# Kernel optimization log

Hardware: AMD Instinct MI355X
Metric: run time of the kernel (lower is better)

Reference implementation:

```python
import jax, jax.numpy as jnp
import numpy as np

B, L, IN_DIM, D_MODEL = 4, 1024, 128, 256
MDIM = 2 * D_MODEL          # mamba_dim = 512 (must equal 2*d_model for shape consistency)
NL = 4                      # mamba_layers
DIN = 2 * MDIM              # d_inner (expand=2)
NST = 16                    # d_state
DTR = MDIM // 16            # dt_rank = 32
KC = 4                      # d_conv
EPS = 1e-5

# sinusoidal positional encoding buffer (deterministic)
_pos = np.arange(L, dtype=np.float32)[:, None]
_div = np.exp(np.arange(0, MDIM, 2, dtype=np.float32) * (-np.log(10000.0) / MDIM))
_pe = np.zeros((L, MDIM), dtype=np.float32)
_pe[:, 0::2] = np.sin(_pos * _div)
_pe[:, 1::2] = np.cos(_pos * _div)
PE = jnp.asarray(_pe)


def setup_inputs() -> dict:
    key = jax.random.key(0)
    ks = iter(jax.random.split(key, 64))
    rn = lambda shape, s=0.02: jax.random.normal(next(ks), shape, jnp.float32) * s
    inp = {
        "x": jax.random.normal(next(ks), (B, L, IN_DIM), jnp.float32),
        "rtg": jax.random.normal(next(ks), (B, L, 1), jnp.float32),
        "state_emb_w": rn((D_MODEL, IN_DIM)), "state_emb_b": jnp.zeros((D_MODEL,)),
        "reward_emb_w": rn((D_MODEL, 1)), "reward_emb_b": jnp.zeros((D_MODEL,)),
        "ln_w": jnp.ones((MDIM,)), "ln_b": jnp.zeros((MDIM,)),
        "in_proj_w": rn((NL, 2 * DIN, MDIM)),
        "conv_w": rn((NL, DIN, KC), 0.1), "conv_b": jnp.zeros((NL, DIN)),
        "x_proj_w": rn((NL, DTR + 2 * NST, DIN)),
        "dt_proj_w": rn((NL, DIN, DTR), 0.1), "dt_proj_b": jnp.full((NL, DIN), -2.0),
        "A_log": jnp.tile(jnp.log(jnp.arange(1, NST + 1, dtype=jnp.float32)), (NL, DIN, 1)),
        "D_param": jnp.ones((NL, DIN)),
        "out_proj_w": rn((NL, MDIM, DIN)),
        "norm_w": jnp.ones((NL, MDIM)), "norm_f_w": jnp.ones((MDIM,)),
        "so_w1": rn((MDIM // 2, MDIM)), "so_b1": jnp.zeros((MDIM // 2,)),
        "so_w2": rn((IN_DIM, MDIM // 2)), "so_b2": jnp.zeros((IN_DIM,)),
        "ro_w1": rn((MDIM // 2, MDIM)), "ro_b1": jnp.zeros((MDIM // 2,)),
        "ro_w2": rn((1, MDIM // 2)), "ro_b2": jnp.zeros((1,)),
    }
    return inp


def _rmsnorm(h, w):
    return h * jax.lax.rsqrt(jnp.mean(h * h, -1, keepdims=True) + EPS) * w


def _mamba(h, ipw, cw, cb, xpw, dpw, dpb, Alog, Dp, opw):
    # h: [B,L,MDIM]
    Ls = h.shape[1]
    xz = h @ ipw.T                                   # [B,L,2*DIN]
    xx, z = jnp.split(xz, 2, axis=-1)
    # causal depthwise conv, kernel KC, left pad KC-1
    xp = jnp.pad(xx, ((0, 0), (KC - 1, 0), (0, 0)))
    xc = cb + sum(cw[:, k] * xp[:, k:k + Ls, :] for k in range(KC))
    xc = jax.nn.silu(xc)                             # [B,L,DIN]
    dbc = xc @ xpw.T                                 # [B,L,DTR+2*NST]
    dt = jax.nn.softplus(dbc[..., :DTR] @ dpw.T + dpb)   # [B,L,DIN]
    Bm = dbc[..., DTR:DTR + NST]                     # [B,L,NST]
    Cm = dbc[..., DTR + NST:]                        # [B,L,NST]
    A = -jnp.exp(Alog)                               # [DIN,NST]

    def step(hc, inp):
        dt_t, B_t, C_t, x_t = inp                    # [B,DIN],[B,NST],[B,NST],[B,DIN]
        hc = jnp.exp(dt_t[:, :, None] * A) * hc + (dt_t * x_t)[:, :, None] * B_t[:, None, :]
        return hc, jnp.einsum('bdn,bn->bd', hc, C_t)

    h0 = jnp.zeros((h.shape[0], DIN, NST), h.dtype)
    _, ys = jax.lax.scan(step, h0, (dt.swapaxes(0, 1), Bm.swapaxes(0, 1),
                                    Cm.swapaxes(0, 1), xc.swapaxes(0, 1)))
    y = ys.swapaxes(0, 1) + Dp * xc
    y = y * jax.nn.silu(z)
    return y @ opw.T                                 # [B,L,MDIM]


def _forward(x, rtg, state_emb_w, state_emb_b, reward_emb_w, reward_emb_b, ln_w, ln_b,
             in_proj_w, conv_w, conv_b, x_proj_w, dt_proj_w, dt_proj_b, A_log, D_param,
             out_proj_w, norm_w, norm_f_w, so_w1, so_b1, so_w2, so_b2, ro_w1, ro_b1, ro_w2, ro_b2):
    se = x @ state_emb_w.T + state_emb_b            # [B,L,D_MODEL]
    re = rtg @ reward_emb_w.T + reward_emb_b        # [B,L,D_MODEL]
    h = jnp.concatenate([se, re], axis=-1)          # [B,L,MDIM]
    h = h + PE[:h.shape[1]]                          # dropout is identity at eval
    mu = jnp.mean(h, -1, keepdims=True)
    var = jnp.var(h, -1, keepdims=True)
    h = (h - mu) * jax.lax.rsqrt(var + EPS) * ln_w + ln_b
    residual = None
    for i in range(NL):
        residual = h if residual is None else h + residual
        hn = _rmsnorm(residual, norm_w[i])
        h = _mamba(hn, in_proj_w[i], conv_w[i], conv_b[i], x_proj_w[i],
                   dt_proj_w[i], dt_proj_b[i], A_log[i], D_param[i], out_proj_w[i])
    residual = h + residual
    h = _rmsnorm(residual, norm_f_w)
    next_state = jax.nn.relu(h @ so_w1.T + so_b1) @ so_w2.T + so_b2   # [B,L,IN_DIM]
    next_reward = jax.nn.relu(h @ ro_w1.T + ro_b1) @ ro_w2.T + ro_b2  # [B,L,1]
    return next_state, next_reward


def reference(x, rtg, state_emb_w, state_emb_b, reward_emb_w, reward_emb_b, ln_w, ln_b,
              in_proj_w, conv_w, conv_b, x_proj_w, dt_proj_w, dt_proj_b, A_log, D_param,
              out_proj_w, norm_w, norm_f_w, so_w1, so_b1, so_w2, so_b2, ro_w1, ro_b1, ro_w2, ro_b2):
    return _forward(x, rtg, state_emb_w, state_emb_b, reward_emb_w, reward_emb_b, ln_w, ln_b,
                    in_proj_w, conv_w, conv_b, x_proj_w, dt_proj_w, dt_proj_b, A_log, D_param,
                    out_proj_w, norm_w, norm_f_w, so_w1, so_b1, so_w2, so_b2, ro_w1, ro_b1, ro_w2, ro_b2)
```

## Files before the change

### kernel.cpp

```cpp
#include <hip/hip_runtime.h>
#include <stdint.h>

typedef unsigned short u16;
typedef __attribute__((ext_vector_type(8))) short bf16x8;
typedef __attribute__((ext_vector_type(8))) u16 u16x8;
typedef __attribute__((ext_vector_type(4))) float f32x4;

static __device__ __forceinline__ u16 f2b(float f) {
  uint32_t u = __builtin_bit_cast(uint32_t, f);
  u += 0x7fffu + ((u >> 16) & 1u);
  return (u16)(u >> 16);
}
static __device__ __forceinline__ float b2f(u16 h) {
  uint32_t u = ((uint32_t)h) << 16;
  return __builtin_bit_cast(float, u);
}

#define GLDS16(gsrc, ldst)                                                        \
  __builtin_amdgcn_global_load_lds(                                               \
      (const __attribute__((address_space(1))) void*)(gsrc),                      \
      (__attribute__((address_space(3))) void*)(ldst), 16, 0, 0)

__global__ __launch_bounds__(256) void setup_kernel(
    const float* __restrict__ ipw, u16* __restrict__ ipwb,
    const float* __restrict__ xpw, u16* __restrict__ xpwb,
    const float* __restrict__ opw, u16* __restrict__ opwb,
    const float* __restrict__ sow1, u16* __restrict__ sow1b,
    const float* __restrict__ sow2, u16* __restrict__ sow2b,
    const float* __restrict__ row1, u16* __restrict__ row1b,
    float* __restrict__ PEt,
    const float* __restrict__ dpw, float* __restrict__ dpwT,
    const float* __restrict__ cw, float* __restrict__ cwT) {
  int i = blockIdx.x * 256 + threadIdx.x;
  if (i < 4194304) { ipwb[i] = f2b(ipw[i]); return; } i -= 4194304;
  if (i < 262144)  { xpwb[i] = f2b(xpw[i]); return; } i -= 262144;
  if (i < 2097152) { opwb[i] = f2b(opw[i]); return; } i -= 2097152;
  if (i < 131072)  { sow1b[i] = f2b(sow1[i]); return; } i -= 131072;
  if (i < 32768)   { sow2b[i] = f2b(sow2[i]); return; } i -= 32768;
  if (i < 131072)  { row1b[i] = f2b(row1[i]); return; } i -= 131072;
  if (i < 524288) {
    int dd = i & 511, l = i >> 9;
    const float cc = -9.210340371976184f / 512.f;
    float div = expf((float)(2 * (dd >> 1)) * cc);
    PEt[i] = (dd & 1) ? cosf((float)l * div) : sinf((float)l * div);
    return;
  } i -= 524288;
  if (i < 131072) {
    int l = i >> 15, r = i & 32767, j = r >> 10, dd = r & 1023;
    dpwT[i] = dpw[(size_t)l * 32768 + (size_t)dd * 32 + j];
    return;
  } i -= 131072;
  if (i < 16384) {
    int l = i >> 12, r = i & 4095, k = r >> 10, dd = r & 1023;
    cwT[i] = cw[(size_t)l * 4096 + (size_t)dd * 4 + k];
  }
}

__global__ __launch_bounds__(256) void embed_ln2(
    const float* __restrict__ x, const float* __restrict__ rtg,
    const float* __restrict__ Wse, const float* __restrict__ bse,
    const float* __restrict__ Wre, const float* __restrict__ bre,
    const float* __restrict__ lnw, const float* __restrict__ lnb,
    const float* __restrict__ PEt, float* __restrict__ h) {
  const int tid = threadIdx.x;
  const int tok0 = blockIdx.x * 16;
  const int l0 = tok0 & 1023;
  __shared__ float xs[16][128];
  __shared__ float rt[16];
  __shared__ float sw[16][2][4];
  for (int i = tid; i < 16 * 128; i += 256) ((float*)xs)[i] = x[(size_t)tok0 * 128 + i];
  if (tid < 16) rt[tid] = rtg[tok0 + tid];
  __syncthreads();
  const int d = tid;
  float acc[16];
#pragma unroll
  for (int tt = 0; tt < 16; ++tt) acc[tt] = 0.f;
  const float* wrow = Wse + (size_t)d * 128;
  for (int k0 = 0; k0 < 128; k0 += 8) {
    float4 wa = *(const float4*)(wrow + k0);
    float4 wb = *(const float4*)(wrow + k0 + 4);
#pragma unroll
    for (int tt = 0; tt < 16; ++tt) {
      const float* xr = &xs[tt][k0];
      acc[tt] += xr[0] * wa.x + xr[1] * wa.y + xr[2] * wa.z + xr[3] * wa.w +
                 xr[4] * wb.x + xr[5] * wb.y + xr[6] * wb.z + xr[7] * wb.w;
    }
  }
  const float seb = bse[d], reW = Wre[d], reB = bre[d];
  const int lane = tid & 63, wv = tid >> 6;
  float h1a[16];
#pragma unroll
  for (int tt = 0; tt < 16; ++tt) {
    float h0 = acc[tt] + seb + PEt[(size_t)(l0 + tt) * 512 + d];
    float h1 = reB + rt[tt] * reW + PEt[(size_t)(l0 + tt) * 512 + 256 + d];
    acc[tt] = h0;
    h1a[tt] = h1;
    float s = h0 + h1, q = h0 * h0 + h1 * h1;
#pragma unroll
    for (int o = 32; o; o >>= 1) { s += __shfl_xor(s, o); q += __shfl_xor(q, o); }
    if (lane == 0) { sw[tt][0][wv] = s; sw[tt][1][wv] = q; }
  }
  __syncthreads();
#pragma unroll
  for (int tt = 0; tt < 16; ++tt) {
    float S = sw[tt][0][0] + sw[tt][0][1] + sw[tt][0][2] + sw[tt][0][3];
    float Q = sw[tt][1][0] + sw[tt][1][1] + sw[tt][1][2] + sw[tt][1][3];
    float mean = S * (1.f / 512.f);
    float var = Q * (1.f / 512.f) - mean * mean;
    float rstd = rsqrtf(var + 1e-5f);
    size_t base = (size_t)(tok0 + tt) * 512;
    h[base + d]       = (acc[tt] - mean) * rstd * lnw[d] + lnb[d];
    h[base + 256 + d] = (h1a[tt] - mean) * rstd * lnw[256 + d] + lnb[256 + d];
  }
}

__global__ __launch_bounds__(256) void resid_rms_kernel(
    const float* __restrict__ hin, float* __restrict__ residual,
    const float* __restrict__ w, u16* __restrict__ outb, int first) {
  const int tok = blockIdx.x;
  const int t = threadIdx.x;
  __shared__ float rq[4];
  size_t base = (size_t)tok * 512;
  float v0 = hin[base + t], v1 = hin[base + t + 256];
  if (!first) { v0 += residual[base + t]; v1 += residual[base + t + 256]; }
  residual[base + t] = v0;
  residual[base + t + 256] = v1;
  float q = v0 * v0 + v1 * v1;
#pragma unroll
  for (int o = 32; o; o >>= 1) q += __shfl_xor(q, o);
  if ((t & 63) == 0) rq[t >> 6] = q;
  __syncthreads();
  float Q = rq[0] + rq[1] + rq[2] + rq[3];
  float scale = rsqrtf(Q * (1.f / 512.f) + 1e-5f);
  outb[base + t]       = f2b(v0 * scale * w[t]);
  outb[base + t + 256] = f2b(v1 * scale * w[t + 256]);
}

template <int BM, int BN, int WM, int WN, int EPI>
__global__ __launch_bounds__(256) void gemm_bt(
    const u16* __restrict__ A, const u16* __restrict__ Bw,
    float* __restrict__ Cf, u16* __restrict__ Cb,
    const float* __restrict__ bias, const float* __restrict__ bias2,
    int M, int N, int K, int As) {
  constexpr int MF = BM / (WM * 16);
  constexpr int NF = BN / (WN * 16);
  constexpr int NCA = (BM * 4) / 256;
  constexpr int NCB = (BN * 4) / 256;
  __shared__ __align__(16) u16 lA[BM * 32];
  __shared__ __align__(16) u16 lB[BN * 32];
  const int tid = threadIdx.x;
  const int lane = tid & 63;
  const int wv = tid >> 6;
  const int wr = wv / WN, wc = wv % WN;
  const int m0 = blockIdx.x * BM, n0 = blockIdx.y * BN;
  const int kchunk = K / gridDim.z;
  const int kb = blockIdx.z * kchunk;

  f32x4 acc[MF][NF];
#pragma unroll
  for (int i = 0; i < MF; ++i)
#pragma unroll
    for (int j = 0; j < NF; ++j) acc[i][j] = (f32x4){0.f, 0.f, 0.f, 0.f};

  const int srow = tid >> 2, sck = tid & 3;
  const u16* Ag = A + (size_t)(m0 + srow) * As + sck * 8 + kb;
  const u16* Bg = Bw + (size_t)(n0 + srow) * K + sck * 8 + kb;

  for (int k0 = 0; k0 < kchunk; k0 += 32) {
#pragma unroll
    for (int it = 0; it < NCA; ++it)
      GLDS16(Ag + (size_t)it * 64 * As + k0, &lA[(it * 256 + tid) * 8]);
#pragma unroll
    for (int it = 0; it < NCB; ++it)
      GLDS16(Bg + (size_t)it * 64 * K + k0, &lB[(it * 256 + tid) * 8]);
    __syncthreads();
    bf16x8 af[MF], bfr[NF];
    const int koff = (lane >> 4) * 8;
#pragma unroll
    for (int mi = 0; mi < MF; ++mi) {
      int r = wr * (MF * 16) + mi * 16 + (lane & 15);
      af[mi] = *(const bf16x8*)(&lA[r * 32 + koff]);
    }
#pragma unroll
    for (int ni = 0; ni < NF; ++ni) {
      int r = wc * (NF * 16) + ni * 16 + (lane & 15);
      bfr[ni] = *(const bf16x8*)(&lB[r * 32 + koff]);
    }
#pragma unroll
    for (int mi = 0; mi < MF; ++mi)
#pragma unroll
      for (int ni = 0; ni < NF; ++ni)
        acc[mi][ni] = __builtin_amdgcn_mfma_f32_16x16x32_bf16(af[mi], bfr[ni], acc[mi][ni], 0, 0, 0);
    __syncthreads();
  }

  float* co = Cf + (size_t)blockIdx.z * (size_t)M * N;
  const int rbase = (lane >> 4) * 4;
  const int cbase = lane & 15;
#pragma unroll
  for (int mi = 0; mi < MF; ++mi) {
#pragma unroll
    for (int ni = 0; ni < NF; ++ni) {
      int row = m0 + wr * (MF * 16) + mi * 16 + rbase;
      int col = n0 + wc * (NF * 16) + ni * 16 + cbase;
      float bv = 0.f;
      if (EPI == 2 || EPI == 3) bv = bias[col];
      if (EPI == 4) bv = (col < 256) ? bias[col] : bias2[col - 256];
#pragma unroll
      for (int r = 0; r < 4; ++r) {
        float v = acc[mi][ni][r] + bv;
        if (EPI == 2 || EPI == 4) v = fmaxf(v, 0.f);
        size_t idx = (size_t)(row + r) * N + col;
        if (EPI == 1 || EPI == 2 || EPI == 4) Cb[idx] = f2b(v);
        else co[idx] = v;
      }
    }
  }
}

__global__ __launch_bounds__(256) void conv_silu_f(
    const u16* __restrict__ xz, const float* __restrict__ cwT,
    const float* __restrict__ cb, float* __restrict__ xcf, u16* __restrict__ xcb) {
  int gid = blockIdx.x * 256 + threadIdx.x;
  int d0 = (gid & 127) * 8;
  int token = gid >> 7;
  int t = token & 1023;
  const u16* xx = xz + (size_t)(token - t) * 2048 + d0;
  float s[8];
  {
    float4 cba = *(const float4*)(cb + d0);
    float4 cbb = *(const float4*)(cb + d0 + 4);
    s[0] = cba.x; s[1] = cba.y; s[2] = cba.z; s[3] = cba.w;
    s[4] = cbb.x; s[5] = cbb.y; s[6] = cbb.z; s[7] = cbb.w;
  }
#pragma unroll
  for (int k = 0; k < 4; ++k) {
    int tt = t - 3 + k;
    if (tt >= 0) {
      u16x8 v = *(const u16x8*)(xx + (size_t)tt * 2048);
      float4 wA = *(const float4*)(cwT + (size_t)k * 1024 + d0);
      float4 wB = *(const float4*)(cwT + (size_t)k * 1024 + d0 + 4);
      s[0] += wA.x * b2f(v[0]); s[1] += wA.y * b2f(v[1]);
      s[2] += wA.z * b2f(v[2]); s[3] += wA.w * b2f(v[3]);
      s[4] += wB.x * b2f(v[4]); s[5] += wB.y * b2f(v[5]);
      s[6] += wB.z * b2f(v[6]); s[7] += wB.w * b2f(v[7]);
    }
  }
  u16x8 o;
  float4 fa, fb;
#pragma unroll
  for (int j = 0; j < 8; ++j) {
    float sl = s[j] / (1.f + expf(-s[j]));
    s[j] = sl;
    o[j] = f2b(sl);
  }
  fa.x = s[0]; fa.y = s[1]; fa.z = s[2]; fa.w = s[3];
  fb.x = s[4]; fb.y = s[5]; fb.z = s[6]; fb.w = s[7];
  *(float4*)(xcf + (size_t)token * 1024 + d0) = fa;
  *(float4*)(xcf + (size_t)token * 1024 + d0 + 4) = fb;
  *(u16x8*)(xcb + (size_t)token * 1024 + d0) = o;
}

__global__ __launch_bounds__(256) void dt_kernel2(
    const float* __restrict__ P, const float* __restrict__ dpwT,
    const float* __restrict__ dpb, float* __restrict__ dtout,
    float* __restrict__ dbcr) {
  const int tid = threadIdx.x;
  const int tok0 = blockIdx.x * 16;
  __shared__ float sm[16][64];
  const size_t str = (size_t)4096 * 64;
  for (int i = tid; i < 16 * 64; i += 256) {
    size_t o = (size_t)tok0 * 64 + i;
    float v = P[o] + P[str + o] + P[2 * str + o] + P[3 * str + o];
    ((float*)sm)[i] = v;
    dbcr[o] = v;
  }
  __syncthreads();
  float acc0[16], acc1[16], acc2[16], acc3[16];
#pragma unroll
  for (int t = 0; t < 16; ++t) { acc0[t] = 0.f; acc1[t] = 0.f; acc2[t] = 0.f; acc3[t] = 0.f; }
#pragma unroll 4
  for (int j = 0; j < 32; ++j) {
    float w0 = dpwT[(size_t)j * 1024 + tid];
    float w1 = dpwT[(size_t)j * 1024 + 256 + tid];
    float w2 = dpwT[(size_t)j * 1024 + 512 + tid];
    float w3 = dpwT[(size_t)j * 1024 + 768 + tid];
#pragma unroll
    for (int t = 0; t < 16; ++t) {
      float sv = sm[t][j];
      acc0[t] += sv * w0;
      acc1[t] += sv * w1;
      acc2[t] += sv * w2;
      acc3[t] += sv * w3;
    }
  }
  const float b0 = dpb[tid], b1 = dpb[256 + tid], b2 = dpb[512 + tid], b3 = dpb[768 + tid];
#pragma unroll
  for (int t = 0; t < 16; ++t) {
    size_t o = (size_t)(tok0 + t) * 1024 + tid;
    float a0 = acc0[t] + b0, a1 = acc1[t] + b1, a2 = acc2[t] + b2, a3 = acc3[t] + b3;
    dtout[o]       = (a0 > 20.f) ? a0 : logf(1.f + expf(a0));
    dtout[o + 256] = (a1 > 20.f) ? a1 : logf(1.f + expf(a1));
    dtout[o + 512] = (a2 > 20.f) ? a2 : logf(1.f + expf(a2));
    dtout[o + 768] = (a3 > 20.f) ? a3 : logf(1.f + expf(a3));
  }
}

__global__ __launch_bounds__(256) void scan1(
    const float* __restrict__ dt, const float* __restrict__ xc,
    const float* __restrict__ dbc, const float* __restrict__ Alog,
    float* __restrict__ Ebuf, float* __restrict__ Ubuf, int NCc, int TCc) {
  const int d = blockIdx.x * 256 + threadIdx.x;
  const int c = blockIdx.y;
  const int b = blockIdx.z;
  const int t0 = c * TCc;
  __shared__ __align__(16) float sB[64][16];
  for (int i = threadIdx.x; i < TCc * 16; i += 256) {
    int t = i >> 4, n = i & 15;
    sB[t][n] = dbc[((size_t)(b * 1024 + t0 + t)) * 64 + 32 + n];
  }
  float A2[16];
#pragma unroll
  for (int q = 0; q < 4; ++q) {
    float4 a4 = *(const float4*)(Alog + (size_t)d * 16 + q * 4);
    A2[q * 4 + 0] = -expf(a4.x) * 1.4426950408889634f;
    A2[q * 4 + 1] = -expf(a4.y) * 1.4426950408889634f;
    A2[q * 4 + 2] = -expf(a4.z) * 1.4426950408889634f;
    A2[q * 4 + 3] = -expf(a4.w) * 1.4426950408889634f;
  }
  __syncthreads();
  float hc[16];
#pragma unroll
  for (int n = 0; n < 16; ++n) hc[n] = 0.f;
  float sumdt = 0.f;
  size_t tok = (size_t)b * 1024 + t0;
  for (int t = 0; t < TCc; ++t, ++tok) {
    float dtv = dt[tok * 1024 + d];
    float xcv = xc[tok * 1024 + d];
    float du = dtv * xcv;
    sumdt += dtv;
#pragma unroll
    for (int q = 0; q < 4; ++q) {
      float4 B4 = *(const float4*)(&sB[t][q * 4]);
      float e0 = exp2f(dtv * A2[q * 4 + 0]);
      float e1 = exp2f(dtv * A2[q * 4 + 1]);
      float e2 = exp2f(dtv * A2[q * 4 + 2]);
      float e3 = exp2f(dtv * A2[q * 4 + 3]);
      hc[q * 4 + 0] = e0 * hc[q * 4 + 0] + du * B4.x;
      hc[q * 4 + 1] = e1 * hc[q * 4 + 1] + du * B4.y;
      hc[q * 4 + 2] = e2 * hc[q * 4 + 2] + du * B4.z;
      hc[q * 4 + 3] = e3 * hc[q * 4 + 3] + du * B4.w;
    }
  }
  size_t ob = (((size_t)b * NCc + c) * 16) * 1024 + d;
#pragma unroll
  for (int n = 0; n < 16; ++n) {
    Ebuf[ob + (size_t)n * 1024] = exp2f(A2[n] * sumdt);
    Ubuf[ob + (size_t)n * 1024] = hc[n];
  }
}

__global__ __launch_bounds__(256) void scan_mid(
    const float* __restrict__ Ebuf, const float* __restrict__ Ubuf,
    float* __restrict__ H0, int NCc) {
  int idx = blockIdx.x * 256 + threadIdx.x;
  int b = idx >> 14;
  int nd = idx & 16383;
  float h = 0.f;
  size_t o0 = ((size_t)b * NCc * 16) * 1024 + nd;
  const size_t cstr = (size_t)16 * 1024;
  for (int cc = 0; cc < NCc; ++cc) {
    size_t o = o0 + (size_t)cc * cstr;
    H0[o] = h;
    if (cc < NCc - 1) h = Ebuf[o] * h + Ubuf[o];
  }
}

__global__ __launch_bounds__(256) void scan2(
    const float* __restrict__ dt, const float* __restrict__ xc,
    const float* __restrict__ dbc, const u16* __restrict__ xz,
    const float* __restrict__ Alog, const float* __restrict__ Dp,
    const float* __restrict__ H0, u16* __restrict__ yg, int NCc, int TCc) {
  const int d = blockIdx.x * 256 + threadIdx.x;
  const int c = blockIdx.y;
  const int b = blockIdx.z;
  const int t0 = c * TCc;
  __shared__ __align__(16) float sB[64][16];
  __shared__ __align__(16) float sC[64][16];
  for (int i = threadIdx.x; i < TCc * 16; i += 256) {
    int t = i >> 4, n = i & 15;
    size_t o = ((size_t)(b * 1024 + t0 + t)) * 64 + 32;
    sB[t][n] = dbc[o + n];
    sC[t][n] = dbc[o + 16 + n];
  }
  float A2[16];
#pragma unroll
  for (int q = 0; q < 4; ++q) {
    float4 a4 = *(const float4*)(Alog + (size_t)d * 16 + q * 4);
    A2[q * 4 + 0] = -expf(a4.x) * 1.4426950408889634f;
    A2[q * 4 + 1] = -expf(a4.y) * 1.4426950408889634f;
    A2[q * 4 + 2] = -expf(a4.z) * 1.4426950408889634f;
    A2[q * 4 + 3] = -expf(a4.w) * 1.4426950408889634f;
  }
  const float Dd = Dp[d];
  float hc[16];
  size_t ob = (((size_t)b * NCc + c) * 16) * 1024 + d;
#pragma unroll
  for (int n = 0; n < 16; ++n) hc[n] = H0[ob + (size_t)n * 1024];
  __syncthreads();
  size_t tok = (size_t)b * 1024 + t0;
  for (int t = 0; t < TCc; ++t, ++tok) {
    float dtv = dt[tok * 1024 + d];
    float xcv = xc[tok * 1024 + d];
    float du = dtv * xcv;
    float y0 = 0.f, y1 = 0.f, y2 = 0.f, y3 = 0.f;
#pragma unroll
    for (int q = 0; q < 4; ++q) {
      float4 B4 = *(const float4*)(&sB[t][q * 4]);
      float4 C4 = *(const float4*)(&sC[t][q * 4]);
      float e0 = exp2f(dtv * A2[q * 4 + 0]);
      float e1 = exp2f(dtv * A2[q * 4 + 1]);
      float e2 = exp2f(dtv * A2[q * 4 + 2]);
      float e3 = exp2f(dtv * A2[q * 4 + 3]);
      hc[q * 4 + 0] = e0 * hc[q * 4 + 0] + du * B4.x;
      hc[q * 4 + 1] = e1 * hc[q * 4 + 1] + du * B4.y;
      hc[q * 4 + 2] = e2 * hc[q * 4 + 2] + du * B4.z;
      hc[q * 4 + 3] = e3 * hc[q * 4 + 3] + du * B4.w;
      y0 += hc[q * 4 + 0] * C4.x;
      y1 += hc[q * 4 + 1] * C4.y;
      y2 += hc[q * 4 + 2] * C4.z;
      y3 += hc[q * 4 + 3] * C4.w;
    }
    float y = (y0 + y1) + (y2 + y3);
    float z = b2f(xz[tok * 2048 + 1024 + d]);
    float g = z / (1.f + expf(-z));
    yg[tok * 1024 + d] = f2b((y + Dd * xcv) * g);
  }
}

__global__ __launch_bounds__(256) void reward_head_kernel(
    const u16* __restrict__ t1sr, const float* __restrict__ w2,
    const float* __restrict__ b2, float* __restrict__ outr) {
  int tok = blockIdx.x * 4 + (threadIdx.x >> 6);
  int lane = threadIdx.x & 63;
  float s = 0.f;
#pragma unroll
  for (int j = 0; j < 256; j += 64)
    s += b2f(t1sr[(size_t)tok * 512 + 256 + j + lane]) * w2[j + lane];
#pragma unroll
  for (int o = 32; o; o >>= 1) s += __shfl_xor(s, o);
  if (lane == 0) outr[tok] = s + b2[0];
}

extern "C" void kernel_launch(void* const* d_in, const int* in_sizes, int n_in,
                              void* d_out, int out_size, void* d_ws, size_t ws_size,
                              hipStream_t stream) {
  const float* x    = (const float*)d_in[0];
  const float* rtg  = (const float*)d_in[1];
  const float* Wse  = (const float*)d_in[2];
  const float* bse  = (const float*)d_in[3];
  const float* Wre  = (const float*)d_in[4];
  const float* bre  = (const float*)d_in[5];
  const float* lnw  = (const float*)d_in[6];
  const float* lnb  = (const float*)d_in[7];
  const float* ipw  = (const float*)d_in[8];
  const float* cw   = (const float*)d_in[9];
  const float* cb   = (const float*)d_in[10];
  const float* xpw  = (const float*)d_in[11];
  const float* dpw  = (const float*)d_in[12];
  const float* dpb  = (const float*)d_in[13];
  const float* Alog = (const float*)d_in[14];
  const float* Dp   = (const float*)d_in[15];
  const float* opw  = (const float*)d_in[16];
  const float* nw   = (const float*)d_in[17];
  const float* nfw  = (const float*)d_in[18];
  const float* sow1 = (const float*)d_in[19];
  const float* sob1 = (const float*)d_in[20];
  const float* sow2 = (const float*)d_in[21];
  const float* sob2 = (const float*)d_in[22];
  const float* row1 = (const float*)d_in[23];
  const float* rob1 = (const float*)d_in[24];
  const float* row2 = (const float*)d_in[25];
  const float* rob2 = (const float*)d_in[26];
  (void)in_sizes; (void)n_in; (void)out_size;

  char* wsp = (char*)d_ws;
  size_t off = 0;
  auto alloc = [&](size_t bytes) -> void* {
    off = (off + 255) & ~(size_t)255;
    void* p = wsp + off;
    off += bytes;
    return p;
  };
  const int TOK = 4096;
  float* h     = (float*)alloc((size_t)TOK * 512 * 4);
  float* resid = (float*)alloc((size_t)TOK * 512 * 4);
  u16* hn      = (u16*)alloc((size_t)TOK * 512 * 2);
  u16* xzb     = (u16*)alloc((size_t)TOK * 2048 * 2);
  float* xcf   = (float*)alloc((size_t)TOK * 1024 * 4);
  u16* xcb     = (u16*)alloc((size_t)TOK * 1024 * 2);
  float* dbcP  = (float*)alloc((size_t)4 * TOK * 64 * 4);
  float* dbc   = (float*)alloc((size_t)TOK * 64 * 4);
  float* dtf   = (float*)alloc((size_t)TOK * 1024 * 4);
  float* PEt   = (float*)alloc((size_t)1024 * 512 * 4);
  float* dpwT  = (float*)alloc((size_t)4 * 32 * 1024 * 4);
  float* cwT   = (float*)alloc((size_t)4 * 4 * 1024 * 4);
  u16* ipwb    = (u16*)alloc((size_t)4 * 2048 * 512 * 2);
  u16* xpwb    = (u16*)alloc((size_t)4 * 64 * 1024 * 2);
  u16* opwb    = (u16*)alloc((size_t)4 * 512 * 1024 * 2);
  u16* sow1b   = (u16*)alloc((size_t)256 * 512 * 2);
  u16* row1b   = (u16*)alloc((size_t)256 * 512 * 2);
  u16* sow2b   = (u16*)alloc((size_t)128 * 256 * 2);

  size_t base_off = (off + 255) & ~(size_t)255;
  auto scan_bytes = [](int nc) {
    return (size_t)3 * 4 * nc * 16 * 1024 * 4 + 512;
  };
  int NCc = 16;
  if (ws_size >= base_off + scan_bytes(64)) NCc = 64;
  else if (ws_size >= base_off + scan_bytes(32)) NCc = 32;
  int TCc = 1024 / NCc;
  char* shared8 = (char*)alloc((size_t)2 * 4096 * NCc * 16 * 4);
  float* Ebuf  = (float*)shared8;
  float* Ubuf  = Ebuf + (size_t)4096 * NCc * 16;
  float* H0    = (float*)alloc((size_t)4096 * NCc * 16 * 4);
  u16* t1sr    = (u16*)shared8;

  setup_kernel<<<29376, 256, 0, stream>>>(ipw, ipwb, xpw, xpwb, opw, opwb,
                                          sow1, sow1b, sow2, sow2b, row1, row1b,
                                          PEt, dpw, dpwT, cw, cwT);
  embed_ln2<<<256, 256, 0, stream>>>(x, rtg, Wse, bse, Wre, bre, lnw, lnb, PEt, h);

  for (int i = 0; i < 4; ++i) {
    resid_rms_kernel<<<TOK, 256, 0, stream>>>(h, resid, nw + i * 512, hn, i == 0);
    gemm_bt<128, 128, 2, 2, 1><<<dim3(32, 16, 1), 256, 0, stream>>>(
        hn, ipwb + (size_t)i * 2048 * 512, nullptr, xzb, nullptr, nullptr,
        4096, 2048, 512, 512);
    conv_silu_f<<<2048, 256, 0, stream>>>(
        xzb, cwT + (size_t)i * 4096, cb + i * 1024, xcf, xcb);
    gemm_bt<128, 64, 2, 2, 0><<<dim3(32, 1, 4), 256, 0, stream>>>(
        xcb, xpwb + (size_t)i * 64 * 1024, dbcP, nullptr, nullptr, nullptr,
        4096, 64, 1024, 1024);
    dt_kernel2<<<TOK / 16, 256, 0, stream>>>(dbcP, dpwT + (size_t)i * 32 * 1024,
                                             dpb + i * 1024, dtf, dbc);
    scan1<<<dim3(4, NCc - 1, 4), 256, 0, stream>>>(
        dtf, xcf, dbc, Alog + (size_t)i * 1024 * 16, Ebuf, Ubuf, NCc, TCc);
    scan_mid<<<256, 256, 0, stream>>>(Ebuf, Ubuf, H0, NCc);
    scan2<<<dim3(4, NCc, 4), 256, 0, stream>>>(
        dtf, xcf, dbc, xzb, Alog + (size_t)i * 1024 * 16, Dp + i * 1024,
        H0, xcb, NCc, TCc);
    gemm_bt<128, 64, 2, 2, 0><<<dim3(32, 8, 1), 256, 0, stream>>>(
        xcb, opwb + (size_t)i * 512 * 1024, h, nullptr, nullptr, nullptr,
        4096, 512, 1024, 1024);
  }

  resid_rms_kernel<<<TOK, 256, 0, stream>>>(h, resid, nfw, hn, 0);
  gemm_bt<64, 64, 2, 2, 4><<<dim3(64, 8, 1), 256, 0, stream>>>(
      hn, sow1b, nullptr, t1sr, sob1, rob1, 4096, 512, 512, 512);
  gemm_bt<64, 64, 2, 2, 3><<<dim3(64, 2, 1), 256, 0, stream>>>(
      t1sr, sow2b, (float*)d_out, nullptr, sob2, nullptr, 4096, 128, 256, 512);
  reward_head_kernel<<<TOK / 4, 256, 0, stream>>>(
      t1sr, row2, rob2, (float*)d_out + (size_t)TOK * 128);
}
```

Measured before the change: 673.0 us.

## Precompute A2 table, replace Ebuf with per-chunk dt sums, retile small GEMMs

Precomputes -exp(A_log)*log2e once in the setup kernel, stored transposed so the scan kernels load it coalesced instead of recomputing expf. scan1 now writes only the per-chunk dt sum rather than a full 16-state decay buffer, and scan_mid recomputes the decay with exp2f, cutting scan intermediate traffic. The x_proj GEMM uses 64x64 tiles with split-K of 8 (8 partials summed in dt_kernel2), and out_proj uses 64x64 tiles for more blocks. This trades extra partial-sum traffic and some recomputed exponentials for better occupancy and less memory traffic.

```diff
diff --git a/kernel.cpp b/kernel.cpp
--- a/kernel.cpp
+++ b/kernel.cpp
@@ -30,7 +30,8 @@
     const float* __restrict__ row1, u16* __restrict__ row1b,
     float* __restrict__ PEt,
     const float* __restrict__ dpw, float* __restrict__ dpwT,
-    const float* __restrict__ cw, float* __restrict__ cwT) {
+    const float* __restrict__ cw, float* __restrict__ cwT,
+    const float* __restrict__ Alog, float* __restrict__ A2T) {
   int i = blockIdx.x * 256 + threadIdx.x;
   if (i < 4194304) { ipwb[i] = f2b(ipw[i]); return; } i -= 4194304;
   if (i < 262144)  { xpwb[i] = f2b(xpw[i]); return; } i -= 262144;
@@ -53,6 +54,11 @@
   if (i < 16384) {
     int l = i >> 12, r = i & 4095, k = r >> 10, dd = r & 1023;
     cwT[i] = cw[(size_t)l * 4096 + (size_t)dd * 4 + k];
+    return;
+  } i -= 16384;
+  if (i < 65536) {
+    int l = i >> 14, r = i & 16383, n = r >> 10, d = r & 1023;
+    A2T[i] = -expf(Alog[(size_t)l * 16384 + (size_t)d * 16 + n]) * 1.4426950408889634f;
   }
 }
 
@@ -271,7 +277,9 @@
   const size_t str = (size_t)4096 * 64;
   for (int i = tid; i < 16 * 64; i += 256) {
     size_t o = (size_t)tok0 * 64 + i;
-    float v = P[o] + P[str + o] + P[2 * str + o] + P[3 * str + o];
+    float v = 0.f;
+#pragma unroll
+    for (int p = 0; p < 8; ++p) v += P[(size_t)p * str + o];
     ((float*)sm)[i] = v;
     dbcr[o] = v;
   }
@@ -308,8 +316,8 @@
 
 __global__ __launch_bounds__(256) void scan1(
     const float* __restrict__ dt, const float* __restrict__ xc,
-    const float* __restrict__ dbc, const float* __restrict__ Alog,
-    float* __restrict__ Ebuf, float* __restrict__ Ubuf, int NCc, int TCc) {
+    const float* __restrict__ dbc, const float* __restrict__ A2T_l,
+    float* __restrict__ Ubuf, float* __restrict__ SD, int NCc, int TCc) {
   const int d = blockIdx.x * 256 + threadIdx.x;
   const int c = blockIdx.y;
   const int b = blockIdx.z;
@@ -321,13 +329,7 @@
   }
   float A2[16];
 #pragma unroll
-  for (int q = 0; q < 4; ++q) {
-    float4 a4 = *(const float4*)(Alog + (size_t)d * 16 + q * 4);
-    A2[q * 4 + 0] = -expf(a4.x) * 1.4426950408889634f;
-    A2[q * 4 + 1] = -expf(a4.y) * 1.4426950408889634f;
-    A2[q * 4 + 2] = -expf(a4.z) * 1.4426950408889634f;
-    A2[q * 4 + 3] = -expf(a4.w) * 1.4426950408889634f;
-  }
+  for (int n = 0; n < 16; ++n) A2[n] = A2T_l[(size_t)n * 1024 + d];
   __syncthreads();
   float hc[16];
 #pragma unroll
@@ -354,32 +356,36 @@
   }
   size_t ob = (((size_t)b * NCc + c) * 16) * 1024 + d;
 #pragma unroll
-  for (int n = 0; n < 16; ++n) {
-    Ebuf[ob + (size_t)n * 1024] = exp2f(A2[n] * sumdt);
-    Ubuf[ob + (size_t)n * 1024] = hc[n];
-  }
+  for (int n = 0; n < 16; ++n) Ubuf[ob + (size_t)n * 1024] = hc[n];
+  SD[((size_t)b * NCc + c) * 1024 + d] = sumdt;
 }
 
 __global__ __launch_bounds__(256) void scan_mid(
-    const float* __restrict__ Ebuf, const float* __restrict__ Ubuf,
-    float* __restrict__ H0, int NCc) {
+    const float* __restrict__ Ubuf, const float* __restrict__ SD,
+    const float* __restrict__ A2T_l, float* __restrict__ H0, int NCc) {
   int idx = blockIdx.x * 256 + threadIdx.x;
   int b = idx >> 14;
   int nd = idx & 16383;
+  int d = nd & 1023;
+  const float A2 = A2T_l[nd];
   float h = 0.f;
   size_t o0 = ((size_t)b * NCc * 16) * 1024 + nd;
   const size_t cstr = (size_t)16 * 1024;
+  size_t sd0 = ((size_t)b * NCc) * 1024 + d;
   for (int cc = 0; cc < NCc; ++cc) {
     size_t o = o0 + (size_t)cc * cstr;
     H0[o] = h;
-    if (cc < NCc - 1) h = Ebuf[o] * h + Ubuf[o];
+    if (cc < NCc - 1) {
+      float e = exp2f(A2 * SD[sd0 + (size_t)cc * 1024]);
+      h = e * h + Ubuf[o];
+    }
   }
 }
 
 __global__ __launch_bounds__(256) void scan2(
     const float* __restrict__ dt, const float* __restrict__ xc,
     const float* __restrict__ dbc, const u16* __restrict__ xz,
-    const float* __restrict__ Alog, const float* __restrict__ Dp,
+    const float* __restrict__ A2T_l, const float* __restrict__ Dp,
     const float* __restrict__ H0, u16* __restrict__ yg, int NCc, int TCc) {
   const int d = blockIdx.x * 256 + threadIdx.x;
   const int c = blockIdx.y;
@@ -395,13 +401,7 @@
   }
   float A2[16];
 #pragma unroll
-  for (int q = 0; q < 4; ++q) {
-    float4 a4 = *(const float4*)(Alog + (size_t)d * 16 + q * 4);
-    A2[q * 4 + 0] = -expf(a4.x) * 1.4426950408889634f;
-    A2[q * 4 + 1] = -expf(a4.y) * 1.4426950408889634f;
-    A2[q * 4 + 2] = -expf(a4.z) * 1.4426950408889634f;
-    A2[q * 4 + 3] = -expf(a4.w) * 1.4426950408889634f;
-  }
+  for (int n = 0; n < 16; ++n) A2[n] = A2T_l[(size_t)n * 1024 + d];
   const float Dd = Dp[d];
   float hc[16];
   size_t ob = (((size_t)b * NCc + c) * 16) * 1024 + d;
@@ -499,12 +499,13 @@
   u16* xzb     = (u16*)alloc((size_t)TOK * 2048 * 2);
   float* xcf   = (float*)alloc((size_t)TOK * 1024 * 4);
   u16* xcb     = (u16*)alloc((size_t)TOK * 1024 * 2);
-  float* dbcP  = (float*)alloc((size_t)4 * TOK * 64 * 4);
+  float* dbcP  = (float*)alloc((size_t)8 * TOK * 64 * 4);
   float* dbc   = (float*)alloc((size_t)TOK * 64 * 4);
   float* dtf   = (float*)alloc((size_t)TOK * 1024 * 4);
   float* PEt   = (float*)alloc((size_t)1024 * 512 * 4);
   float* dpwT  = (float*)alloc((size_t)4 * 32 * 1024 * 4);
   float* cwT   = (float*)alloc((size_t)4 * 4 * 1024 * 4);
+  float* A2T   = (float*)alloc((size_t)4 * 16 * 1024 * 4);
   u16* ipwb    = (u16*)alloc((size_t)4 * 2048 * 512 * 2);
   u16* xpwb    = (u16*)alloc((size_t)4 * 64 * 1024 * 2);
   u16* opwb    = (u16*)alloc((size_t)4 * 512 * 1024 * 2);
@@ -514,42 +515,41 @@
 
   size_t base_off = (off + 255) & ~(size_t)255;
   auto scan_bytes = [](int nc) {
-    return (size_t)3 * 4 * nc * 16 * 1024 * 4 + 512;
+    return (size_t)2 * 4 * nc * 16 * 1024 * 4 + (size_t)4 * nc * 1024 * 4 + 1024;
   };
   int NCc = 16;
   if (ws_size >= base_off + scan_bytes(64)) NCc = 64;
   else if (ws_size >= base_off + scan_bytes(32)) NCc = 32;
   int TCc = 1024 / NCc;
-  char* shared8 = (char*)alloc((size_t)2 * 4096 * NCc * 16 * 4);
-  float* Ebuf  = (float*)shared8;
-  float* Ubuf  = Ebuf + (size_t)4096 * NCc * 16;
+  float* Ubuf  = (float*)alloc((size_t)4096 * NCc * 16 * 4);
   float* H0    = (float*)alloc((size_t)4096 * NCc * 16 * 4);
-  u16* t1sr    = (u16*)shared8;
-
-  setup_kernel<<<29376, 256, 0, stream>>>(ipw, ipwb, xpw, xpwb, opw, opwb,
+  float* SD    = (float*)alloc((size_t)4 * NCc * 1024 * 4);
+  u16* t1sr    = (u16*)Ubuf;
+
+  setup_kernel<<<29632, 256, 0, stream>>>(ipw, ipwb, xpw, xpwb, opw, opwb,
                                           sow1, sow1b, sow2, sow2b, row1, row1b,
-                                          PEt, dpw, dpwT, cw, cwT);
+                                          PEt, dpw, dpwT, cw, cwT, Alog, A2T);
   embed_ln2<<<256, 256, 0, stream>>>(x, rtg, Wse, bse, Wre, bre, lnw, lnb, PEt, h);
 
   for (int i = 0; i < 4; ++i) {
+    const float* A2Tl = A2T + (size_t)i * 16 * 1024;
     resid_rms_kernel<<<TOK, 256, 0, stream>>>(h, resid, nw + i * 512, hn, i == 0);
     gemm_bt<128, 128, 2, 2, 1><<<dim3(32, 16, 1), 256, 0, stream>>>(
         hn, ipwb + (size_t)i * 2048 * 512, nullptr, xzb, nullptr, nullptr,
         4096, 2048, 512, 512);
     conv_silu_f<<<2048, 256, 0, stream>>>(
         xzb, cwT + (size_t)i * 4096, cb + i * 1024, xcf, xcb);
-    gemm_bt<128, 64, 2, 2, 0><<<dim3(32, 1, 4), 256, 0, stream>>>(
+    gemm_bt<64, 64, 2, 2, 0><<<dim3(64, 1, 8), 256, 0, stream>>>(
         xcb, xpwb + (size_t)i * 64 * 1024, dbcP, nullptr, nullptr, nullptr,
         4096, 64, 1024, 1024);
     dt_kernel2<<<TOK / 16, 256, 0, stream>>>(dbcP, dpwT + (size_t)i * 32 * 1024,
                                              dpb + i * 1024, dtf, dbc);
     scan1<<<dim3(4, NCc - 1, 4), 256, 0, stream>>>(
-        dtf, xcf, dbc, Alog + (size_t)i * 1024 * 16, Ebuf, Ubuf, NCc, TCc);
-    scan_mid<<<256, 256, 0, stream>>>(Ebuf, Ubuf, H0, NCc);
+        dtf, xcf, dbc, A2Tl, Ubuf, SD, NCc, TCc);
+    scan_mid<<<256, 256, 0, stream>>>(Ubuf, SD, A2Tl, H0, NCc);
     scan2<<<dim3(4, NCc, 4), 256, 0, stream>>>(
-        dtf, xcf, dbc, xzb, Alog + (size_t)i * 1024 * 16, Dp + i * 1024,
-        H0, xcb, NCc, TCc);
-    gemm_bt<128, 64, 2, 2, 0><<<dim3(32, 8, 1), 256, 0, stream>>>(
+        dtf, xcf, dbc, xzb, A2Tl, Dp + i * 1024, H0, xcb, NCc, TCc);
+    gemm_bt<64, 64, 2, 2, 0><<<dim3(64, 8, 1), 256, 0, stream>>>(
         xcb, opwb + (size_t)i * 512 * 1024, h, nullptr, nullptr, nullptr,
         4096, 512, 1024, 1024);
   }
```

Measured after the change: 649.2 us. 3.5% less time.
